# Kernel optimization log

Measured on AMD Instinct MI355X. Metric: run time of the kernel, lower is better.

Reference implementation:

```python
import jax, jax.numpy as jnp
import numpy as np

E = 8        # num_local_experts
H = 1024     # hidden_dim
F = 4096     # intermediate_dim
T = 16384    # total permuted tokens (sum of tokens_per_expert)


def setup_inputs() -> dict:
    key = jax.random.key(0)
    k_x, k_w1, k_w2 = jax.random.split(key, 3)
    x = jax.random.normal(k_x, (T, H), dtype=jnp.float32)
    # Ragged tokens-per-expert summing exactly to T (variable group sizes).
    rng = np.random.default_rng(0)
    bounds = np.sort(rng.integers(0, T, size=E - 1))
    counts = np.diff(np.concatenate([[0], bounds, [T]])).astype(np.int32)
    tokens_per_expert = jnp.asarray(counts)  # [E], int32, sums to T
    # xavier_normal_ init per expert matrix: std = sqrt(2/(fan_in+fan_out))
    std = (2.0 / (H + F)) ** 0.5
    weight1 = jax.random.normal(k_w1, (E, H, F), dtype=jnp.float32) * std  # fc1
    weight2 = jax.random.normal(k_w2, (E, F, H), dtype=jnp.float32) * std  # fc2
    return {
        "permuted_local_hidden_states": x,
        "weight1": weight1,
        "weight2": weight2,
        "tokens_per_expert": tokens_per_expert,
    }


def reference(permuted_local_hidden_states, weight1, weight2, tokens_per_expert):
    # Grouped GEMM: rows of x are grouped contiguously by expert; group e uses
    # weight[e]. lax.ragged_dot is the exact analogue of gg.ops.gmm(trans_b=False).
    fc1 = jax.lax.ragged_dot(permuted_local_hidden_states, weight1,
                             tokens_per_expert)            # [T, F]
    act = jax.nn.gelu(fc1, approximate=False)               # activation fused between GEMMs
    fc2 = jax.lax.ragged_dot(act, weight2, tokens_per_expert)  # [T, H]
    return fc2
```

## Files before the change

kernel.cpp:

```cpp
#include <hip/hip_runtime.h>
#include <hip/hip_bf16.h>

#define E_NUM 8
#define H_DIM 1024
#define F_DIM 4096
#define T_TOK 16384

#define NT 256
#define MT_MAX (T_TOK / 128 + E_NUM)
#define MT256 (T_TOK / 256 + E_NUM)

typedef __attribute__((ext_vector_type(8))) short bf16x8;
typedef __attribute__((ext_vector_type(4))) float f32x4;

__device__ __forceinline__ short f2bf(float f) {
    unsigned u = __builtin_bit_cast(unsigned, f);
    u += 0x7FFFu + ((u >> 16) & 1u);
    return (short)(u >> 16);
}

__device__ __forceinline__ float exp2_fast(float a) {
#if __has_builtin(__builtin_amdgcn_exp2f)
    return __builtin_amdgcn_exp2f(a);
#else
    return exp2f(a);
#endif
}
__device__ __forceinline__ float rcp_fast(float a) {
#if __has_builtin(__builtin_amdgcn_rcpf)
    return __builtin_amdgcn_rcpf(a);
#else
    return 1.0f / a;
#endif
}

__device__ __forceinline__ float fast_gelu(float x) {
    float x2 = x * x;
    float y = x * (0.7978845608f + 0.0356774081f * x2);
    float z = exp2_fast(y * 2.8853900817779268f);
    float r = rcp_fast(z + 1.0f);
    return x * (1.0f - r);
}

__device__ __forceinline__ void gload16(const void* g, void* l) {
    __builtin_amdgcn_global_load_lds(
        (const __attribute__((address_space(1))) void*)g,
        (__attribute__((address_space(3))) void*)l, 16, 0, 0);
}

template<int N>
__device__ __forceinline__ void vmwait() {
    if constexpr (N == 0) asm volatile("s_waitcnt vmcnt(0)" ::: "memory");
    else if constexpr (N == 1) asm volatile("s_waitcnt vmcnt(1)" ::: "memory");
    else if constexpr (N == 2) asm volatile("s_waitcnt vmcnt(2)" ::: "memory");
    else if constexpr (N == 3) asm volatile("s_waitcnt vmcnt(3)" ::: "memory");
    else if constexpr (N == 4) asm volatile("s_waitcnt vmcnt(4)" ::: "memory");
}

__device__ __forceinline__ void bar() {
    asm volatile("s_barrier" ::: "memory");
}

__device__ __forceinline__ void tile_map128(const int* __restrict__ cnt, int mt,
                                            int& row0, int& rend, int& e_out) {
    int acc = 0, off = 0;
    e_out = -1;
    for (int i = 0; i < E_NUM; ++i) {
        int c = cnt[i];
        int nti = (c + 127) >> 7;
        if (mt < acc + nti) {
            e_out = i; row0 = off + (mt - acc) * 128; rend = off + c; return;
        }
        acc += nti; off += c;
    }
}

__device__ __forceinline__ void tile_map256(const int* __restrict__ cnt, int mt,
                                            int& row0, int& rend, int& e_out) {
    int acc = 0, off = 0;
    e_out = -1;
    for (int i = 0; i < E_NUM; ++i) {
        int c = cnt[i];
        int nti = (c + 255) >> 8;
        if (mt < acc + nti) {
            e_out = i; row0 = off + (mt - acc) * 256; rend = off + c; return;
        }
        acc += nti; off += c;
    }
}

__global__ __launch_bounds__(NT)
void cvt_x_kernel(const float* __restrict__ in, short* __restrict__ out, int n8) {
    int i = blockIdx.x * blockDim.x + threadIdx.x;
    const int stride = gridDim.x * blockDim.x;
    for (; i < n8; i += stride) {
        f32x4 f0 = ((const f32x4*)in)[(size_t)i * 2];
        f32x4 f1 = ((const f32x4*)in)[(size_t)i * 2 + 1];
        bf16x8 v;
        v[0] = f2bf(f0[0]); v[1] = f2bf(f0[1]); v[2] = f2bf(f0[2]); v[3] = f2bf(f0[3]);
        v[4] = f2bf(f1[0]); v[5] = f2bf(f1[1]); v[6] = f2bf(f1[2]); v[7] = f2bf(f1[3]);
        ((bf16x8*)out)[i] = v;
    }
}

__global__ __launch_bounds__(NT)
void transpose_cvt(const float* __restrict__ in, short* __restrict__ out,
                   int R, int C) {
    __shared__ short tb[64][72];
    const int e = blockIdx.z;
    const float* ine = in + (size_t)e * R * C;
    short* oute = out + (size_t)e * R * C;
    const int c0 = blockIdx.x * 64, r0 = blockIdx.y * 64;
    const int t = threadIdx.x;
    const int rl = t >> 4, cl = (t & 15) * 4;
#pragma unroll
    for (int p = 0; p < 4; ++p) {
        int r = rl + p * 16;
        f32x4 f = *(const f32x4*)(ine + (size_t)(r0 + r) * C + c0 + cl);
#pragma unroll
        for (int j = 0; j < 4; ++j) tb[cl + j][r] = f2bf(f[j]);
    }
    __syncthreads();
    const int c2 = t >> 3, rc = (t & 7) * 8;
#pragma unroll
    for (int p = 0; p < 2; ++p) {
        int c = c2 + p * 32;
        bf16x8 v = *(const bf16x8*)&tb[c][rc];
        *(bf16x8*)(oute + (size_t)(c0 + c) * R + r0 + rc) = v;
    }
}

#define G8P_READ_A(mh)                                                        \
    _Pragma("unroll") for (int f = 0; f < 4; ++f) {                           \
        const int r_ = ((mh) * 4 + f) * 32 + wm * 16 + lr;                    \
        _Pragma("unroll") for (int kk = 0; kk < 2; ++kk) {                    \
            const int u_ = (r_ * 8 + kk * 4 + lg) ^ (r_ & 7);                 \
            areg[f][kk] = ((const bf16x8*)Ac)[u_];                            \
        }                                                                     \
    }

#define G8P_READ_B(nh, BPTR)                                                  \
    _Pragma("unroll") for (int g = 0; g < 2; ++g) {                           \
        const int r_ = ((nh) * 2 + g) * 64 + wn * 16 + lr;                    \
        _Pragma("unroll") for (int kk = 0; kk < 2; ++kk) {                    \
            const int u_ = (r_ * 8 + kk * 4 + lg) ^ (r_ & 7);                 \
            breg[nh][g][kk] = ((const bf16x8*)(BPTR))[u_];                    \
        }                                                                     \
    }

#define G8P_QUAD(mh, nh)                                                      \
    _Pragma("unroll") for (int f = 0; f < 4; ++f)                             \
    _Pragma("unroll") for (int g = 0; g < 2; ++g)                             \
    _Pragma("unroll") for (int kk = 0; kk < 2; ++kk)                          \
        acc[(mh) * 4 + f][(nh) * 2 + g] =                                     \
            __builtin_amdgcn_mfma_f32_16x16x32_bf16(                          \
                areg[f][kk], breg[nh][g][kk],                                 \
                acc[(mh) * 4 + f][(nh) * 2 + g], 0, 0, 0);

template<bool GELU, int LDC, int NTX, int KTOT>
__global__ __launch_bounds__(512, 2)
void gemm8p(const short* __restrict__ A, const short* __restrict__ Bw,
            const int* __restrict__ cnt, void* __restrict__ Cout) {
    constexpr int A_SH = 16384;
    constexpr int SEG = 32768;
    constexpr int KT = KTOT / 64;

    __shared__ __align__(16) short lds[2 * SEG];

    const int lin = blockIdx.x;
    constexpr int CPX = (NTX * MT256) / 8;
    const int wg = (lin & 7) * CPX + (lin >> 3);
    const int mt = wg / NTX;
    const int nt = wg - mt * NTX;

    int row0, rend, e;
    tile_map256(cnt, mt, row0, rend, e);
    if (e < 0) return;
    const int n0 = nt * 256;
    const short* Be = Bw + (size_t)e * ((size_t)F_DIM * H_DIM);

    const int tid = threadIdx.x;
    const int lane = tid & 63;
    const int lr = lane & 15;
    const int lg = lane >> 4;
    const int w = tid >> 6;
    const int wm = w >> 2;
    const int wn = w & 3;

    const short* ag[4];
    const short* bg[4];
#pragma unroll
    for (int p = 0; p < 4; ++p) {
        int s = p * 512 + tid;
        int r = s >> 3;
        int kc = (s & 7) ^ (r & 7);
        int grow = row0 + r;
        if (grow >= T_TOK) grow = T_TOK - 1;
        ag[p] = A + (size_t)grow * KTOT + kc * 8;
        bg[p] = Be + (size_t)(n0 + r) * KTOT + kc * 8;
    }

    f32x4 acc[8][4];
#pragma unroll
    for (int i = 0; i < 8; ++i)
#pragma unroll
        for (int j = 0; j < 4; ++j) acc[i][j] = (f32x4){0.f, 0.f, 0.f, 0.f};
    bf16x8 areg[4][2];
    bf16x8 breg[2][2][2];

    {
        short* An = lds;
        short* Bn = lds + A_SH;
        gload16(ag[0], An + (0 * 512 + tid) * 8); ag[0] += 64;
        gload16(ag[1], An + (1 * 512 + tid) * 8); ag[1] += 64;
        gload16(bg[0], Bn + (0 * 512 + tid) * 8); bg[0] += 64;
        gload16(bg[1], Bn + (1 * 512 + tid) * 8); bg[1] += 64;
        gload16(bg[2], Bn + (2 * 512 + tid) * 8); bg[2] += 64;
        gload16(bg[3], Bn + (3 * 512 + tid) * 8); bg[3] += 64;
        gload16(ag[2], An + (2 * 512 + tid) * 8); ag[2] += 64;
        gload16(ag[3], An + (3 * 512 + tid) * 8); ag[3] += 64;
    }
    vmwait<4>();
    bar();
    G8P_READ_B(0, lds + A_SH)

    int cur = 0;
    for (int kt = 0; kt < KT - 1; ++kt) {
        const short* Ac = lds + cur * SEG;
        const short* Bc = Ac + A_SH;
        short* An = lds + (cur ^ 1) * SEG;
        short* Bn = An + A_SH;

        G8P_READ_A(0)
        gload16(ag[0], An + (0 * 512 + tid) * 8); ag[0] += 64;
        gload16(ag[1], An + (1 * 512 + tid) * 8); ag[1] += 64;
        vmwait<4>();
        bar();
        __builtin_amdgcn_s_setprio(1);
        G8P_QUAD(0, 0)
        __builtin_amdgcn_s_setprio(0);

        G8P_READ_B(1, Bc)
        gload16(bg[0], Bn + (0 * 512 + tid) * 8); bg[0] += 64;
        gload16(bg[1], Bn + (1 * 512 + tid) * 8); bg[1] += 64;
        vmwait<4>();
        bar();
        __builtin_amdgcn_s_setprio(1);
        G8P_QUAD(0, 1)
        __builtin_amdgcn_s_setprio(0);

        G8P_READ_A(1)
        gload16(bg[2], Bn + (2 * 512 + tid) * 8); bg[2] += 64;
        gload16(bg[3], Bn + (3 * 512 + tid) * 8); bg[3] += 64;
        bar();
        __builtin_amdgcn_s_setprio(1);
        G8P_QUAD(1, 1)
        __builtin_amdgcn_s_setprio(0);

        gload16(ag[2], An + (2 * 512 + tid) * 8); ag[2] += 64;
        gload16(ag[3], An + (3 * 512 + tid) * 8); ag[3] += 64;
        vmwait<4>();
        bar();
        __builtin_amdgcn_s_setprio(1);
        G8P_QUAD(1, 0)
        __builtin_amdgcn_s_setprio(0);
        G8P_READ_B(0, Bn)
        cur ^= 1;
    }

    {
        const short* Ac = lds + cur * SEG;
        const short* Bc = Ac + A_SH;
        G8P_READ_A(0)
        vmwait<2>();
        bar();
        G8P_QUAD(0, 0)
        G8P_READ_B(1, Bc)
        vmwait<0>();
        bar();
        G8P_QUAD(0, 1)
        G8P_READ_A(1)
        G8P_QUAD(1, 1)
        G8P_QUAD(1, 0)
    }

#pragma unroll
    for (int f = 0; f < 8; ++f) {
#pragma unroll
        for (int g = 0; g < 4; ++g) {
            const int gcol = n0 + g * 64 + wn * 16 + lr;
#pragma unroll
            for (int rr = 0; rr < 4; ++rr) {
                const int grow = row0 + f * 32 + wm * 16 + lg * 4 + rr;
                if (grow < rend) {
                    float v = acc[f][g][rr];
                    if constexpr (GELU) {
                        ((short*)Cout)[(size_t)grow * LDC + gcol] = f2bf(fast_gelu(v));
                    } else {
                        ((float*)Cout)[(size_t)grow * LDC + gcol] = v;
                    }
                }
            }
        }
    }
}

__global__ __launch_bounds__(NT)
void gemm1_kernel(const float* __restrict__ X, const float* __restrict__ W1,
                  const int* __restrict__ cnt, short* __restrict__ act) {
    __shared__ short Alds[128 * 64];
    __shared__ short Blds[128 * 64];

    int row0, rend, e;
    tile_map128(cnt, blockIdx.y, row0, rend, e);
    if (e < 0) return;

    const int n0 = blockIdx.x * 128;
    const float* W = W1 + (size_t)e * H_DIM * F_DIM;

    const int tid = threadIdx.x;
    const int lane = tid & 63;
    const int w = tid >> 6;
    const int wr = (w >> 1) * 64;
    const int wc = (w & 1) * 64;
    const int lr = lane & 15;
    const int lg = lane >> 4;

    const int a_r0 = tid >> 3;
    const int a_kc = tid & 7;
    const int b_n = tid & 127;
    const int b_kg = (tid >> 7) * 8;

    f32x4 acc[4][4];
#pragma unroll
    for (int i = 0; i < 4; ++i)
#pragma unroll
        for (int j = 0; j < 4; ++j) acc[i][j] = (f32x4){0.f, 0.f, 0.f, 0.f};

    for (int kt = 0; kt < H_DIM / 64; ++kt) {
        const int k0 = kt * 64;
#pragma unroll
        for (int p = 0; p < 4; ++p) {
            int r = a_r0 + 32 * p;
            int grow = row0 + r;
            if (grow > T_TOK - 1) grow = T_TOK - 1;
            const float* src = X + (size_t)grow * H_DIM + k0 + a_kc * 8;
            f32x4 f0 = *(const f32x4*)src;
            f32x4 f1 = *(const f32x4*)(src + 4);
            bf16x8 v;
            v[0] = f2bf(f0[0]); v[1] = f2bf(f0[1]); v[2] = f2bf(f0[2]); v[3] = f2bf(f0[3]);
            v[4] = f2bf(f1[0]); v[5] = f2bf(f1[1]); v[6] = f2bf(f1[2]); v[7] = f2bf(f1[3]);
            ((bf16x8*)Alds)[(r * 8 + a_kc) ^ (r & 7)] = v;
        }
#pragma unroll
        for (int p = 0; p < 4; ++p) {
            int kb = p * 16 + b_kg;
            const float* src = W + (size_t)(k0 + kb) * F_DIM + n0 + b_n;
            bf16x8 v;
#pragma unroll
            for (int j = 0; j < 8; ++j) v[j] = f2bf(src[(size_t)j * F_DIM]);
            ((bf16x8*)Blds)[(b_n * 8 + (kb >> 3)) ^ (b_n & 7)] = v;
        }
        __syncthreads();
#pragma unroll
        for (int kk = 0; kk < 2; ++kk) {
            bf16x8 af[4], bfr[4];
#pragma unroll
            for (int fm = 0; fm < 4; ++fm) {
                int r = wr + fm * 16 + lr;
                af[fm] = ((bf16x8*)Alds)[(r * 8 + kk * 4 + lg) ^ (r & 7)];
            }
#pragma unroll
            for (int fn = 0; fn < 4; ++fn) {
                int n = wc + fn * 16 + lr;
                bfr[fn] = ((bf16x8*)Blds)[(n * 8 + kk * 4 + lg) ^ (n & 7)];
            }
#pragma unroll
            for (int fm = 0; fm < 4; ++fm)
#pragma unroll
                for (int fn = 0; fn < 4; ++fn)
                    acc[fm][fn] = __builtin_amdgcn_mfma_f32_16x16x32_bf16(
                        af[fm], bfr[fn], acc[fm][fn], 0, 0, 0);
        }
        __syncthreads();
    }

#pragma unroll
    for (int fm = 0; fm < 4; ++fm)
#pragma unroll
        for (int fn = 0; fn < 4; ++fn) {
            int gcol = n0 + wc + fn * 16 + lr;
#pragma unroll
            for (int rr = 0; rr < 4; ++rr) {
                int grow = row0 + wr + fm * 16 + lg * 4 + rr;
                if (grow < rend)
                    act[(size_t)grow * F_DIM + gcol] = f2bf(fast_gelu(acc[fm][fn][rr]));
            }
        }
}

__global__ __launch_bounds__(NT)
void gemm2_kernel(const short* __restrict__ ACT, const float* __restrict__ W2,
                  const int* __restrict__ cnt, float* __restrict__ out) {
    __shared__ short Alds[128 * 64];
    __shared__ short Blds[128 * 64];

    int row0, rend, e;
    tile_map128(cnt, blockIdx.y, row0, rend, e);
    if (e < 0) return;

    const int n0 = blockIdx.x * 128;
    const float* W = W2 + (size_t)e * F_DIM * H_DIM;

    const int tid = threadIdx.x;
    const int lane = tid & 63;
    const int w = tid >> 6;
    const int wr = (w >> 1) * 64;
    const int wc = (w & 1) * 64;
    const int lr = lane & 15;
    const int lg = lane >> 4;

    const int a_r0 = tid >> 3;
    const int a_kc = tid & 7;
    const int b_n = tid & 127;
    const int b_kg = (tid >> 7) * 8;

    f32x4 acc[4][4];
#pragma unroll
    for (int i = 0; i < 4; ++i)
#pragma unroll
        for (int j = 0; j < 4; ++j) acc[i][j] = (f32x4){0.f, 0.f, 0.f, 0.f};

    for (int kt = 0; kt < F_DIM / 64; ++kt) {
        const int k0 = kt * 64;
#pragma unroll
        for (int p = 0; p < 4; ++p) {
            int r = a_r0 + 32 * p;
            int grow = row0 + r;
            if (grow > T_TOK - 1) grow = T_TOK - 1;
            bf16x8 v = *(const bf16x8*)(ACT + (size_t)grow * F_DIM + k0 + a_kc * 8);
            ((bf16x8*)Alds)[(r * 8 + a_kc) ^ (r & 7)] = v;
        }
#pragma unroll
        for (int p = 0; p < 4; ++p) {
            int kb = p * 16 + b_kg;
            const float* src = W + (size_t)(k0 + kb) * H_DIM + n0 + b_n;
            bf16x8 v;
#pragma unroll
            for (int j = 0; j < 8; ++j) v[j] = f2bf(src[(size_t)j * H_DIM]);
            ((bf16x8*)Blds)[(b_n * 8 + (kb >> 3)) ^ (b_n & 7)] = v;
        }
        __syncthreads();
#pragma unroll
        for (int kk = 0; kk < 2; ++kk) {
            bf16x8 af[4], bfr[4];
#pragma unroll
            for (int fm = 0; fm < 4; ++fm) {
                int r = wr + fm * 16 + lr;
                af[fm] = ((bf16x8*)Alds)[(r * 8 + kk * 4 + lg) ^ (r & 7)];
            }
#pragma unroll
            for (int fn = 0; fn < 4; ++fn) {
                int n = wc + fn * 16 + lr;
                bfr[fn] = ((bf16x8*)Blds)[(n * 8 + kk * 4 + lg) ^ (n & 7)];
            }
#pragma unroll
            for (int fm = 0; fm < 4; ++fm)
#pragma unroll
                for (int fn = 0; fn < 4; ++fn)
                    acc[fm][fn] = __builtin_amdgcn_mfma_f32_16x16x32_bf16(
                        af[fm], bfr[fn], acc[fm][fn], 0, 0, 0);
        }
        __syncthreads();
    }

#pragma unroll
    for (int fm = 0; fm < 4; ++fm)
#pragma unroll
        for (int fn = 0; fn < 4; ++fn) {
            int gcol = n0 + wc + fn * 16 + lr;
#pragma unroll
            for (int rr = 0; rr < 4; ++rr) {
                int grow = row0 + wr + fm * 16 + lg * 4 + rr;
                if (grow < rend) out[(size_t)grow * H_DIM + gcol] = acc[fm][fn][rr];
            }
        }
}

extern "C" void kernel_launch(void* const* d_in, const int* in_sizes, int n_in,
                              void* d_out, int out_size, void* d_ws, size_t ws_size,
                              hipStream_t stream) {
    const float* x  = (const float*)d_in[0];
    const float* w1 = (const float*)d_in[1];
    const float* w2 = (const float*)d_in[2];
    const int* cnt  = (const int*)d_in[3];
    float* out = (float*)d_out;

    const size_t ACT_B = (size_t)T_TOK * F_DIM * 2;
    const size_t WT_B  = (size_t)E_NUM * F_DIM * H_DIM * 2;
    const size_t XB_B  = (size_t)T_TOK * H_DIM * 2;

    if (ws_size >= ACT_B + WT_B + XB_B) {
        short* act = (short*)d_ws;
        short* wt  = (short*)((char*)d_ws + ACT_B);
        short* xb  = (short*)((char*)d_ws + ACT_B + WT_B);

        cvt_x_kernel<<<2048, NT, 0, stream>>>(x, xb, T_TOK * H_DIM / 8);
        transpose_cvt<<<dim3(F_DIM / 64, H_DIM / 64, E_NUM), NT, 0, stream>>>(
            w1, wt, H_DIM, F_DIM);
        gemm8p<true, F_DIM, 16, H_DIM>
            <<<16 * MT256, 512, 0, stream>>>(xb, wt, cnt, (void*)act);
        transpose_cvt<<<dim3(H_DIM / 64, F_DIM / 64, E_NUM), NT, 0, stream>>>(
            w2, wt, F_DIM, H_DIM);
        gemm8p<false, H_DIM, 4, F_DIM>
            <<<4 * MT256, 512, 0, stream>>>(act, wt, cnt, (void*)out);
    } else if (ws_size >= ACT_B) {
        short* act = (short*)d_ws;
        gemm1_kernel<<<dim3(F_DIM / 128, MT_MAX), NT, 0, stream>>>(x, w1, cnt, act);
        gemm2_kernel<<<dim3(H_DIM / 128, MT_MAX), NT, 0, stream>>>(act, w2, cnt, out);
    }
}
```

Before: 465.7 us.

## Split-K the second grouped GEMM with atomics and remap tiles into supertiles

```diff
diff --git a/kernel.cpp b/kernel.cpp
--- a/kernel.cpp
+++ b/kernel.cpp
@@ -9,6 +9,7 @@
 #define NT 256
 #define MT_MAX (T_TOK / 128 + E_NUM)
 #define MT256 (T_TOK / 256 + E_NUM)
+static_assert(MT256 % 8 == 0, "supertile remap needs MT256 % 8 == 0");
 
 typedef __attribute__((ext_vector_type(8))) short bf16x8;
 typedef __attribute__((ext_vector_type(4))) float f32x4;
@@ -157,21 +158,31 @@
                 areg[f][kk], breg[nh][g][kk],                                 \
                 acc[(mh) * 4 + f][(nh) * 2 + g], 0, 0, 0);
 
-template<bool GELU, int LDC, int NTX, int KTOT>
+template<bool GELU, int LDC, int NTX, int LDK, int KSPLIT>
 __global__ __launch_bounds__(512, 2)
 void gemm8p(const short* __restrict__ A, const short* __restrict__ Bw,
             const int* __restrict__ cnt, void* __restrict__ Cout) {
     constexpr int A_SH = 16384;
     constexpr int SEG = 32768;
-    constexpr int KT = KTOT / 64;
+    constexpr int KEXT = LDK / KSPLIT;
+    constexpr int KT = KEXT / 64;
+    constexpr bool ATOMIC = (KSPLIT > 1);
 
     __shared__ __align__(16) short lds[2 * SEG];
 
+    constexpr int TOT = KSPLIT * NTX * MT256;
+    static_assert(TOT % 8 == 0, "grid must be divisible by 8 XCDs");
+    constexpr int CPX = TOT / 8;
     const int lin = blockIdx.x;
-    constexpr int CPX = (NTX * MT256) / 8;
-    const int wg = (lin & 7) * CPX + (lin >> 3);
-    const int mt = wg / NTX;
-    const int nt = wg - mt * NTX;
+    int wg = (lin & 7) * CPX + (lin >> 3);
+
+    const int ks = wg / (NTX * MT256);
+    wg -= ks * (NTX * MT256);
+
+    const int stripe = wg / (8 * NTX);
+    const int within = wg - stripe * (8 * NTX);
+    const int mt = stripe * 8 + (within & 7);
+    const int nt = within >> 3;
 
     int row0, rend, e;
     tile_map256(cnt, mt, row0, rend, e);
@@ -196,8 +207,8 @@
         int kc = (s & 7) ^ (r & 7);
         int grow = row0 + r;
         if (grow >= T_TOK) grow = T_TOK - 1;
-        ag[p] = A + (size_t)grow * KTOT + kc * 8;
-        bg[p] = Be + (size_t)(n0 + r) * KTOT + kc * 8;
+        ag[p] = A + (size_t)grow * LDK + ks * KEXT + kc * 8;
+        bg[p] = Be + (size_t)(n0 + r) * LDK + ks * KEXT + kc * 8;
     }
 
     f32x4 acc[8][4];
@@ -296,6 +307,8 @@
                     float v = acc[f][g][rr];
                     if constexpr (GELU) {
                         ((short*)Cout)[(size_t)grow * LDC + gcol] = f2bf(fast_gelu(v));
+                    } else if constexpr (ATOMIC) {
+                        atomicAdd(((float*)Cout) + (size_t)grow * LDC + gcol, v);
                     } else {
                         ((float*)Cout)[(size_t)grow * LDC + gcol] = v;
                     }
@@ -508,12 +521,13 @@
         cvt_x_kernel<<<2048, NT, 0, stream>>>(x, xb, T_TOK * H_DIM / 8);
         transpose_cvt<<<dim3(F_DIM / 64, H_DIM / 64, E_NUM), NT, 0, stream>>>(
             w1, wt, H_DIM, F_DIM);
-        gemm8p<true, F_DIM, 16, H_DIM>
+        gemm8p<true, F_DIM, 16, H_DIM, 1>
             <<<16 * MT256, 512, 0, stream>>>(xb, wt, cnt, (void*)act);
         transpose_cvt<<<dim3(H_DIM / 64, F_DIM / 64, E_NUM), NT, 0, stream>>>(
             w2, wt, F_DIM, H_DIM);
-        gemm8p<false, H_DIM, 4, F_DIM>
-            <<<4 * MT256, 512, 0, stream>>>(act, wt, cnt, (void*)out);
+        hipMemsetAsync(d_out, 0, (size_t)T_TOK * H_DIM * sizeof(float), stream);
+        gemm8p<false, H_DIM, 4, F_DIM, 2>
+            <<<2 * 4 * MT256, 512, 0, stream>>>(act, wt, cnt, (void*)out);
     } else if (ws_size >= ACT_B) {
         short* act = (short*)d_ws;
         gemm1_kernel<<<dim3(F_DIM / 128, MT_MAX), NT, 0, stream>>>(x, w1, cnt, act);
```

Measured after the change: 508.6 us. 1.09x slower.
